# Kernel optimization log

Measured on AMD Instinct MI355X. Metric: run time of the kernel, lower is better.

## Reference

```python
import jax, jax.numpy as jnp
import numpy as np

N = 100000   # num_nodes
H = 128      # hidden_dim
B = 512      # events per forward (batch_size)
D = 32       # fixed neighbor count (padded neighbor list replaces torch.nonzero(A[u]))
NEG = 5      # num_neg_samples
TD_MAX = 1.0 # train_td_max


def setup_inputs() -> dict:
    key = jax.random.key(0)
    ks = jax.random.split(key, 24)
    s = 1.0 / np.sqrt(H)
    inp = {
        # event-stream data (the `data` tuple of forward)
        "time_bar": jax.random.uniform(ks[0], (B, N), dtype=jnp.float32),
        "time_cur": jax.random.uniform(ks[1], (B,), dtype=jnp.float32) + 1.0,
        "time_delta": jax.random.uniform(ks[2], (B, 2), dtype=jnp.float32),
        "u": jax.random.randint(ks[3], (B,), 0, N),
        "neighbors": jax.random.randint(ks[4], (B, D), 0, N),
        "neg_nodes": jax.random.randint(ks[5], (B, NEG), 0, N),
        # recurrent state
        "z0": 0.1 * jax.random.normal(ks[6], (N, H), dtype=jnp.float32),
        # parameters (Linear stored as [in,out] + bias)
        "W_omega": s * jax.random.normal(ks[7], (H,), dtype=jnp.float32),
        "b_omega": jnp.zeros((), jnp.float32),
        "W_h": s * jax.random.normal(ks[8], (H, H), dtype=jnp.float32),
        "b_h": jnp.zeros((H,), jnp.float32),
        "W_e2n": s * jax.random.normal(ks[9], (H, H), dtype=jnp.float32),
        "b_e2n": jnp.zeros((H,), jnp.float32),
        "W_rec_e": s * jax.random.normal(ks[10], (H, H), dtype=jnp.float32),
        "b_rec_e": jnp.zeros((H,), jnp.float32),
        "W_rec_n": s * jax.random.normal(ks[11], (H, H), dtype=jnp.float32),
        "b_rec_n": jnp.zeros((H,), jnp.float32),
        "W_time": s * jax.random.normal(ks[12], (H,), dtype=jnp.float32),
        "b_time": jnp.zeros((H,), jnp.float32),
        "w_t": jnp.full((), 0.5, jnp.float32),
        "alpha": jnp.full((), 0.5, jnp.float32),
        "psi": jnp.full((), 0.5, jnp.float32),
    }
    return inp


def _hawkes(z_u, td, W_omega, b_omega, w_t, alpha, psi):
    # g = omega(z_u); lambda = psi * softplus((g + alpha*exp(-w_t*td)) / psi)
    g = z_u @ W_omega + b_omega                       # [n]
    g = g + alpha * jnp.exp(-w_t * (td / TD_MAX))     # Hawkes time decay
    return psi * jax.nn.softplus(g / psi)             # [n]


def reference(time_bar, time_cur, time_delta, u, neighbors, neg_nodes, z0,
              W_omega, b_omega, W_h, b_h, W_e2n, b_e2n, W_rec_e, b_rec_e,
              W_rec_n, b_rec_n, W_time, b_time, w_t, alpha, psi):
    def step(z, xs):
        u_it, nb_it, tb_it, tc_it, neg_it = xs
        # td for impact nodes: positional indexing into time_bar_it (as in source)
        td = tc_it - tb_it[: 1 + D]                    # [1+D]
        z_u = z[u_it]                                  # [H]  (z_prev row)
        z_nb = z[nb_it]                                # [D,H]
        emb_u = z_u                                    # z_prev[u_event]
        emb_neg = z[neg_it]                            # [NEG,H] z_prev[negatives]
        td_neg = tc_it - tb_it[neg_it]                 # [NEG]
        # recurrent node-embedding update (update_node_embedding_without_attention)
        t_feat = td[:, None] * W_time[None, :] + b_time            # [1+D,H]
        h_u = jax.nn.sigmoid(jnp.mean(z_nb, 0) @ W_h + b_h
                             + z_u @ W_rec_e + b_rec_e + t_feat[0])
        h_nb = jax.nn.sigmoid((z_u @ W_e2n + b_e2n)[None, :]
                              + z_nb @ W_rec_n + b_rec_n + t_feat[1:])
        z = z.at[u_it].set(h_u)
        z = z.at[nb_it].set(h_nb)
        return z, (emb_u, emb_neg, td_neg)

    z_final, (emb_u, emb_neg, td_neg) = jax.lax.scan(
        step, z0, (u, neighbors, time_bar, time_cur, neg_nodes))

    # batch Hawkes intensities on pre-update embeddings
    ts_diff = time_cur - time_delta[:, 0]                           # [B]
    lam = _hawkes(emb_u, ts_diff, W_omega, b_omega, w_t, alpha, psi)          # [B]
    lam_neg = _hawkes(emb_neg.reshape(-1, H), td_neg.reshape(-1),
                      W_omega, b_omega, w_t, alpha, psi)                      # [B*NEG]
    return lam, lam_neg / NEG
```

## Files before the change

kernel.cpp:

```cpp
#include <hip/hip_runtime.h>
#include <stdint.h>

#define NND 100000
#define HD  128
#define BB  512
#define DD  32
#define NNEG 5
#define CAP 12
#define ZROW 132
#define SENT 0xAAAAAAAAu

#define OFF_WCNT     0
#define OFF_WSTEPS   400000
#define OFF_DEP      5200000
#define OFF_STEPOUT  5277824

__global__ void build_writers(const int* __restrict__ u,
                              const int* __restrict__ nb,
                              int* __restrict__ wcnt,
                              int* __restrict__ wsteps) {
    int id = blockIdx.x * blockDim.x + threadIdx.x;
    if (id >= BB * 33) return;
    int s = id / 33, slot = id % 33;
    int row = (slot == 0) ? u[s] : nb[s * DD + slot - 1];
    int pos = atomicAdd(&wcnt[row], 1);
    if (pos < CAP) wsteps[row * CAP + pos] = s * 64 + slot;
}

__global__ void build_deps(const int* __restrict__ u,
                           const int* __restrict__ nb,
                           const int* __restrict__ neg,
                           const int* __restrict__ wcnt,
                           const int* __restrict__ wsteps,
                           int* __restrict__ dep) {
    int id = blockIdx.x * blockDim.x + threadIdx.x;
    if (id >= BB * 38) return;
    int t = id / 38, i = id % 38;
    int row = (i == 0) ? u[t] : (i < 33) ? nb[t * DD + i - 1]
                                         : neg[t * NNEG + i - 33];
    int lim = t * 64;
    int best = -1;
    int n = wcnt[row]; if (n > CAP) n = CAP;
    for (int p = 0; p < n; p++) {
        int e = wsteps[row * CAP + p];
        if (e < lim && e > best) best = e;
    }
    dep[id] = best;
}

__device__ __forceinline__ uint32_t mall_load(const uint32_t* p) {
    return __hip_atomic_load(p, __ATOMIC_RELAXED, __HIP_MEMORY_SCOPE_AGENT);
}
__device__ __forceinline__ void mall_store2(float* p, float v0, float v1) {
    uint64_t pk = ((uint64_t)__float_as_uint(v1) << 32) | (uint64_t)__float_as_uint(v0);
    __hip_atomic_store((unsigned long long*)p, (unsigned long long)pk,
                       __ATOMIC_RELAXED, __HIP_MEMORY_SCOPE_AGENT);
}
__device__ __forceinline__ void flag_set(int* f) {
    __hip_atomic_store(f, 1, __ATOMIC_RELEASE, __HIP_MEMORY_SCOPE_WORKGROUP);
}
__device__ __forceinline__ void flag_wait(int* f) {
    while (__hip_atomic_load(f, __ATOMIC_ACQUIRE, __HIP_MEMORY_SCOPE_WORKGROUP) == 0)
        __builtin_amdgcn_s_sleep(1);
}

__global__ __launch_bounds__(512, 4)
void dyrep_main(const float* __restrict__ time_bar,
                const float* __restrict__ time_cur,
                const float* __restrict__ time_delta,
                const int* __restrict__ u,
                const int* __restrict__ nb,
                const int* __restrict__ neg,
                const float* __restrict__ z0,
                const float* __restrict__ W_omega, const float* __restrict__ b_omega,
                const float* __restrict__ W_h,     const float* __restrict__ b_h,
                const float* __restrict__ W_e2n,   const float* __restrict__ b_e2n,
                const float* __restrict__ W_rec_e, const float* __restrict__ b_rec_e,
                const float* __restrict__ W_rec_n, const float* __restrict__ b_rec_n,
                const float* __restrict__ W_time,  const float* __restrict__ b_time,
                const float* __restrict__ w_t_p,   const float* __restrict__ alpha_p,
                const float* __restrict__ psi_p,
                const int* __restrict__ dep,
                float* __restrict__ step_out,
                float* __restrict__ out) {
    __shared__ float zu[HD];
    __shared__ __align__(16) float znb[DD][ZROW];
    __shared__ float psum[8][HD];
    __shared__ float mbuf[HD];
    __shared__ int flag_zu;
    __shared__ int flag_ps[8];

    const int tid  = threadIdx.x;
    const int lane = tid & 63;
    const int wid  = tid >> 6;
    const int t    = blockIdx.x;
    const int c0   = lane * 2;

    if (tid == 0) flag_zu = 0;
    if (tid < 8)  flag_ps[tid] = 0;
    __syncthreads();

    const float tc  = time_cur[t];
    const float cb0 = b_e2n[c0] + b_rec_n[c0] + b_time[c0];
    const float cb1 = b_e2n[c0+1] + b_rec_n[c0+1] + b_time[c0+1];
    const float wt0 = W_time[c0], wt1 = W_time[c0+1];
    float td_r[4];
    #pragma unroll
    for (int r = 0; r < 4; r++)
        td_r[r] = tc - time_bar[(size_t)t * NND + (1 + 4*wid + r)];

    float cbu0=0.f, cbu1=0.f, td0=0.f, wo0=0.f, wo1=0.f, wt=0.f, al=0.f, ps=0.f, bom=0.f;
    float tdv[6];
    int   negdep[5]; const float* negsrc[5];
    if (wid == 0) {
        cbu0 = b_h[c0] + b_rec_e[c0] + b_time[c0];
        cbu1 = b_h[c0+1] + b_rec_e[c0+1] + b_time[c0+1];
        td0  = tc - time_bar[(size_t)t * NND + 0];
        wo0  = W_omega[c0]; wo1 = W_omega[c0+1];
        wt = *w_t_p; al = *alpha_p; ps = *psi_p; bom = *b_omega;
        tdv[0] = tc - time_delta[t * 2 + 0];
        #pragma unroll
        for (int d = 0; d < 5; d++) {
            int nn = neg[t * NNEG + d];
            tdv[1 + d] = tc - time_bar[(size_t)t * NND + nn];
            int dv = negdep[d] = dep[t * 38 + 33 + d];
            negsrc[d] = (dv >= 0)
                ? step_out + (size_t)(dv >> 6) * 33 * HD + (size_t)(dv & 63) * HD
                : z0 + (size_t)nn * HD;
        }
    }

    if (wid == 0) {
        int d = dep[t * 38 + 0];
        const float* src = (d >= 0)
            ? step_out + (size_t)(d >> 6) * 33 * HD + (size_t)(d & 63) * HD
            : z0 + (size_t)u[t] * HD;
        if (lane < 32) {
            const float* sp = src + lane * 4;
            float4 v;
            if (d >= 0) {
                const uint32_t* ip = (const uint32_t*)sp;
                uint32_t x0, x1, x2, x3;
                while (true) {
                    x0 = mall_load(ip+0); x1 = mall_load(ip+1);
                    x2 = mall_load(ip+2); x3 = mall_load(ip+3);
                    if (x0 != SENT && x1 != SENT && x2 != SENT && x3 != SENT) break;
                    __builtin_amdgcn_s_sleep(1);
                }
                v = make_float4(__uint_as_float(x0), __uint_as_float(x1),
                                __uint_as_float(x2), __uint_as_float(x3));
            } else {
                v = *(const float4*)sp;
            }
            *(float4*)&zu[lane * 4] = v;
        }
        __threadfence_block();
        if (lane == 0) flag_set(&flag_zu);
    }

    {
        const uint32_t* pollp[2]; int lofs[2]; float4 direct[2];
        unsigned pend = 0;
        #pragma unroll
        for (int q = 0; q < 2; q++) {
            int idx = lane + q * 64;
            int rl = idx >> 5, c4 = idx & 31;
            int j = 4 * wid + rl;
            int d = dep[t * 38 + 1 + j];
            const float* sp = (d >= 0)
                ? step_out + (size_t)(d >> 6) * 33 * HD + (size_t)(d & 63) * HD
                : z0 + (size_t)nb[t * DD + j] * HD;
            sp += c4 * 4;
            lofs[q] = j * ZROW + c4 * 4;
            if (d >= 0) { pollp[q] = (const uint32_t*)sp; pend |= (1u << q); }
            else direct[q] = *(const float4*)sp;
        }
        float* zflat = &znb[0][0];
        #pragma unroll
        for (int q = 0; q < 2; q++)
            if (!((pend >> q) & 1)) *(float4*)&zflat[lofs[q]] = direct[q];
        while (__ballot(pend != 0) != 0ULL) {
            #pragma unroll
            for (int q = 0; q < 2; q++) {
                if ((pend >> q) & 1) {
                    const uint32_t* ip = pollp[q];
                    uint32_t x0 = mall_load(ip+0), x1 = mall_load(ip+1);
                    uint32_t x2 = mall_load(ip+2), x3 = mall_load(ip+3);
                    if (x0 != SENT && x1 != SENT && x2 != SENT && x3 != SENT) {
                        *(float4*)&zflat[lofs[q]] =
                            make_float4(__uint_as_float(x0), __uint_as_float(x1),
                                        __uint_as_float(x2), __uint_as_float(x3));
                        pend &= ~(1u << q);
                    }
                }
            }
            if (pend) __builtin_amdgcn_s_sleep(1);
        }
    }
    __threadfence_block();

    {
        float s0 = 0.f, s1 = 0.f;
        #pragma unroll
        for (int r = 0; r < 4; r++) {
            float2 zz = *(const float2*)&znb[4*wid + r][c0];
            s0 += zz.x; s1 += zz.y;
        }
        psum[wid][c0] = s0; psum[wid][c0+1] = s1;
        if (lane == 0) flag_set(&flag_ps[wid]);
        else __builtin_amdgcn_s_sleep(0);
    }

    float2 acc[4];
    #pragma unroll
    for (int r = 0; r < 4; r++) { acc[r].x = 0.f; acc[r].y = 0.f; }
    {
        const float* zr[4];
        #pragma unroll
        for (int r = 0; r < 4; r++) zr[r] = &znb[4*wid + r][0];
        float4 zA[4], zB[4]; float2 wA[4], wB[4];
        #pragma unroll
        for (int r = 0; r < 4; r++) zA[r] = *(const float4*)&zr[r][0];
        #pragma unroll
        for (int kk = 0; kk < 4; kk++) wA[kk] = *(const float2*)&W_rec_n[(size_t)kk * HD + c0];
        for (int kb = 0; kb < HD; kb += 8) {
            #pragma unroll
            for (int r = 0; r < 4; r++) zB[r] = *(const float4*)&zr[r][kb + 4];
            #pragma unroll
            for (int kk = 0; kk < 4; kk++)
                wB[kk] = *(const float2*)&W_rec_n[(size_t)(kb + 4 + kk) * HD + c0];
            #pragma unroll
            for (int r = 0; r < 4; r++) {
                const float za[4] = {zA[r].x, zA[r].y, zA[r].z, zA[r].w};
                #pragma unroll
                for (int kk = 0; kk < 4; kk++) {
                    acc[r].x = fmaf(za[kk], wA[kk].x, acc[r].x);
                    acc[r].y = fmaf(za[kk], wA[kk].y, acc[r].y);
                }
            }
            if (kb + 8 < HD) {
                #pragma unroll
                for (int r = 0; r < 4; r++) zA[r] = *(const float4*)&zr[r][kb + 8];
                #pragma unroll
                for (int kk = 0; kk < 4; kk++)
                    wA[kk] = *(const float2*)&W_rec_n[(size_t)(kb + 8 + kk) * HD + c0];
            }
            #pragma unroll
            for (int r = 0; r < 4; r++) {
                const float zb[4] = {zB[r].x, zB[r].y, zB[r].z, zB[r].w};
                #pragma unroll
                for (int kk = 0; kk < 4; kk++) {
                    acc[r].x = fmaf(zb[kk], wB[kk].x, acc[r].x);
                    acc[r].y = fmaf(zb[kk], wB[kk].y, acc[r].y);
                }
            }
        }
    }

    flag_wait(&flag_zu);
    float e0 = 0.f, e1 = 0.f;
    {
        float4 zA = *(const float4*)&zu[0];
        float2 wA[4], wB[4]; float4 zB;
        #pragma unroll
        for (int kk = 0; kk < 4; kk++) wA[kk] = *(const float2*)&W_e2n[(size_t)kk * HD + c0];
        for (int kb = 0; kb < HD; kb += 8) {
            zB = *(const float4*)&zu[kb + 4];
            #pragma unroll
            for (int kk = 0; kk < 4; kk++)
                wB[kk] = *(const float2*)&W_e2n[(size_t)(kb + 4 + kk) * HD + c0];
            const float za[4] = {zA.x, zA.y, zA.z, zA.w};
            #pragma unroll
            for (int kk = 0; kk < 4; kk++) {
                e0 = fmaf(za[kk], wA[kk].x, e0);
                e1 = fmaf(za[kk], wA[kk].y, e1);
            }
            if (kb + 8 < HD) {
                zA = *(const float4*)&zu[kb + 8];
                #pragma unroll
                for (int kk = 0; kk < 4; kk++)
                    wA[kk] = *(const float2*)&W_e2n[(size_t)(kb + 8 + kk) * HD + c0];
            }
            const float zb[4] = {zB.x, zB.y, zB.z, zB.w};
            #pragma unroll
            for (int kk = 0; kk < 4; kk++) {
                e0 = fmaf(zb[kk], wB[kk].x, e0);
                e1 = fmaf(zb[kk], wB[kk].y, e1);
            }
        }
    }
    float* my_out = step_out + (size_t)t * 33 * HD;
    #pragma unroll
    for (int r = 0; r < 4; r++) {
        int j = 4 * wid + r;
        float p0 = acc[r].x + e0 + td_r[r] * wt0 + cb0;
        float p1 = acc[r].y + e1 + td_r[r] * wt1 + cb1;
        mall_store2(&my_out[(size_t)(1 + j) * HD + c0],
                    1.f / (1.f + __expf(-p0)), 1.f / (1.f + __expf(-p1)));
    }

    if (wid != 0) return;

    #pragma unroll
    for (int g = 0; g < 8; g++) flag_wait(&flag_ps[g]);
    {
        float m0 = 0.f, m1 = 0.f;
        #pragma unroll
        for (int g = 0; g < 8; g++) { m0 += psum[g][c0]; m1 += psum[g][c0+1]; }
        mbuf[c0] = m0 * (1.f/32.f); mbuf[c0+1] = m1 * (1.f/32.f);
    }
    __threadfence_block();
    {
        float a0 = 0.f, a1 = 0.f;
        for (int kb = 0; kb < HD; kb += 4) {
            float4 mv = *(const float4*)&mbuf[kb];
            float4 zv = *(const float4*)&zu[kb];
            const float mm[4] = {mv.x, mv.y, mv.z, mv.w};
            const float zz[4] = {zv.x, zv.y, zv.z, zv.w};
            #pragma unroll
            for (int kk = 0; kk < 4; kk++) {
                float2 wh = *(const float2*)&W_h[(size_t)(kb + kk) * HD + c0];
                float2 wr = *(const float2*)&W_rec_e[(size_t)(kb + kk) * HD + c0];
                a0 = fmaf(mm[kk], wh.x, fmaf(zz[kk], wr.x, a0));
                a1 = fmaf(mm[kk], wh.y, fmaf(zz[kk], wr.y, a1));
            }
        }
        float p0 = a0 + td0 * wt0 + cbu0;
        float p1 = a1 + td0 * wt1 + cbu1;
        mall_store2(&my_out[c0], 1.f / (1.f + __expf(-p0)), 1.f / (1.f + __expf(-p1)));
    }

    {
        float v = zu[c0] * wo0 + zu[c0+1] * wo1;
        #pragma unroll
        for (int off = 32; off; off >>= 1) v += __shfl_down(v, off);
        if (lane == 0) {
            float g = v + bom + al * __expf(-wt * tdv[0]);
            float x = g / ps;
            out[t] = ps * (fmaxf(x, 0.f) + log1pf(__expf(-fabsf(x))));
        }
        for (int d = 0; d < 5; d++) {
            const float* sp = negsrc[d] + c0;
            float x0, x1;
            if (negdep[d] >= 0) {
                const uint32_t* ip = (const uint32_t*)sp;
                uint32_t a, b;
                while (true) {
                    a = mall_load(ip + 0); b = mall_load(ip + 1);
                    if (a != SENT && b != SENT) break;
                    __builtin_amdgcn_s_sleep(1);
                }
                x0 = __uint_as_float(a); x1 = __uint_as_float(b);
            } else {
                x0 = sp[0]; x1 = sp[1];
            }
            float v2 = x0 * wo0 + x1 * wo1;
            #pragma unroll
            for (int off = 32; off; off >>= 1) v2 += __shfl_down(v2, off);
            if (lane == 0) {
                float g = v2 + bom + al * __expf(-wt * tdv[1 + d]);
                float x = g / ps;
                out[BB + t * NNEG + d] =
                    ps * (fmaxf(x, 0.f) + log1pf(__expf(-fabsf(x)))) * (1.0f / NNEG);
            }
        }
    }
}

extern "C" void kernel_launch(void* const* d_in, const int* in_sizes, int n_in,
                              void* d_out, int out_size, void* d_ws, size_t ws_size,
                              hipStream_t stream) {
    const float* time_bar  = (const float*)d_in[0];
    const float* time_cur  = (const float*)d_in[1];
    const float* time_delta= (const float*)d_in[2];
    const int*   u         = (const int*)d_in[3];
    const int*   nb        = (const int*)d_in[4];
    const int*   neg       = (const int*)d_in[5];
    const float* z0        = (const float*)d_in[6];
    const float* W_omega   = (const float*)d_in[7];
    const float* b_omega   = (const float*)d_in[8];
    const float* W_h       = (const float*)d_in[9];
    const float* b_h       = (const float*)d_in[10];
    const float* W_e2n     = (const float*)d_in[11];
    const float* b_e2n     = (const float*)d_in[12];
    const float* W_rec_e   = (const float*)d_in[13];
    const float* b_rec_e   = (const float*)d_in[14];
    const float* W_rec_n   = (const float*)d_in[15];
    const float* b_rec_n   = (const float*)d_in[16];
    const float* W_time    = (const float*)d_in[17];
    const float* b_time    = (const float*)d_in[18];
    const float* w_t       = (const float*)d_in[19];
    const float* alpha     = (const float*)d_in[20];
    const float* psi       = (const float*)d_in[21];

    char* ws = (char*)d_ws;
    int*   wcnt     = (int*)(ws + OFF_WCNT);
    int*   wsteps   = (int*)(ws + OFF_WSTEPS);
    int*   dep      = (int*)(ws + OFF_DEP);
    float* step_out = (float*)(ws + OFF_STEPOUT);
    float* out      = (float*)d_out;

    hipMemsetAsync(ws + OFF_WCNT, 0, NND * 4, stream);
    hipMemsetAsync(ws + OFF_STEPOUT, 0xAA, (size_t)BB * 33 * HD * 4, stream);
    build_writers<<<(BB * 33 + 255) / 256, 256, 0, stream>>>(u, nb, wcnt, wsteps);
    build_deps<<<(BB * 38 + 255) / 256, 256, 0, stream>>>(u, nb, neg, wcnt, wsteps, dep);
    dyrep_main<<<BB, 512, 0, stream>>>(time_bar, time_cur, time_delta, u, nb, neg, z0,
                                       W_omega, b_omega, W_h, b_h, W_e2n, b_e2n,
                                       W_rec_e, b_rec_e, W_rec_n, b_rec_n,
                                       W_time, b_time, w_t, alpha, psi,
                                       dep, step_out, out);
}
```

Measured before the change: 387.9 us.

## Process neighbor rows as they become ready in a polling dataflow loop

Each wave now works through an event loop instead of waiting for all four neighbor rows and z_u before any matvec. Whenever a neighbor row's dependency has been published, the wave runs that row's W_rec_n dot, and it publishes outputs as soon as the W_e2n term is available. This lets downstream blocks start earlier along the dependency chain. The matvecs are also restructured into a shared helper with deeper weight prefetch, at the cost of more registers, per-row weight re-reads (W_rec_n streamed once per row instead of shared across four rows), and more ballot and polling overhead.

```diff
diff --git a/kernel.cpp b/kernel.cpp
--- a/kernel.cpp
+++ b/kernel.cpp
@@ -59,9 +59,44 @@
 __device__ __forceinline__ void flag_set(int* f) {
     __hip_atomic_store(f, 1, __ATOMIC_RELEASE, __HIP_MEMORY_SCOPE_WORKGROUP);
 }
+__device__ __forceinline__ int flag_peek(int* f) {
+    return __hip_atomic_load(f, __ATOMIC_ACQUIRE, __HIP_MEMORY_SCOPE_WORKGROUP);
+}
 __device__ __forceinline__ void flag_wait(int* f) {
-    while (__hip_atomic_load(f, __ATOMIC_ACQUIRE, __HIP_MEMORY_SCOPE_WORKGROUP) == 0)
-        __builtin_amdgcn_s_sleep(1);
+    while (!flag_peek(f)) __builtin_amdgcn_s_sleep(1);
+}
+__device__ __forceinline__ float sigf(float x) {
+    return 1.f / (1.f + __expf(-x));
+}
+
+__device__ __forceinline__ float2 dot_w2(const float* __restrict__ W, int c0,
+                                         const float* __restrict__ zrow) {
+    float a0 = 0.f, a1 = 0.f;
+    float2 wb0[8], wb1[8];
+    #pragma unroll
+    for (int j = 0; j < 8; j++) wb0[j] = *(const float2*)&W[(size_t)j * HD + c0];
+    #pragma unroll
+    for (int kb = 0; kb < HD; kb += 16) {
+        #pragma unroll
+        for (int j = 0; j < 8; j++)
+            wb1[j] = *(const float2*)&W[(size_t)(kb + 8 + j) * HD + c0];
+        #pragma unroll
+        for (int j = 0; j < 8; j++) {
+            float z = zrow[kb + j];
+            a0 = fmaf(z, wb0[j].x, a0); a1 = fmaf(z, wb0[j].y, a1);
+        }
+        if (kb + 16 < HD) {
+            #pragma unroll
+            for (int j = 0; j < 8; j++)
+                wb0[j] = *(const float2*)&W[(size_t)(kb + 16 + j) * HD + c0];
+        }
+        #pragma unroll
+        for (int j = 0; j < 8; j++) {
+            float z = zrow[kb + 8 + j];
+            a0 = fmaf(z, wb1[j].x, a0); a1 = fmaf(z, wb1[j].y, a1);
+        }
+    }
+    return make_float2(a0, a1);
 }
 
 __global__ __launch_bounds__(512, 4)
@@ -101,7 +136,7 @@
     __syncthreads();
 
     const float tc  = time_cur[t];
-    const float cb0 = b_e2n[c0] + b_rec_n[c0] + b_time[c0];
+    const float cb0 = b_e2n[c0]   + b_rec_n[c0]   + b_time[c0];
     const float cb1 = b_e2n[c0+1] + b_rec_n[c0+1] + b_time[c0+1];
     const float wt0 = W_time[c0], wt1 = W_time[c0+1];
     float td_r[4];
@@ -113,7 +148,7 @@
     float tdv[6];
     int   negdep[5]; const float* negsrc[5];
     if (wid == 0) {
-        cbu0 = b_h[c0] + b_rec_e[c0] + b_time[c0];
+        cbu0 = b_h[c0]   + b_rec_e[c0]   + b_time[c0];
         cbu1 = b_h[c0+1] + b_rec_e[c0+1] + b_time[c0+1];
         td0  = tc - time_bar[(size_t)t * NND + 0];
         wo0  = W_omega[c0]; wo1 = W_omega[c0+1];
@@ -130,174 +165,134 @@
         }
     }
 
+    float* zflat = &znb[0][0];
+    const uint32_t* pollp[2]; int lofs[2]; bool done[2];
+    {
+        #pragma unroll
+        for (int q = 0; q < 2; q++) {
+            int rl = q * 2 + (lane >> 5);
+            int j  = 4 * wid + rl;
+            int d  = dep[t * 38 + 1 + j];
+            const float* sp = (d >= 0)
+                ? step_out + (size_t)(d >> 6) * 33 * HD + (size_t)(d & 63) * HD
+                : z0 + (size_t)nb[t * DD + j] * HD;
+            sp += (lane & 31) * 4;
+            lofs[q] = j * ZROW + (lane & 31) * 4;
+            if (d >= 0) { pollp[q] = (const uint32_t*)sp; done[q] = false; }
+            else { *(float4*)&zflat[lofs[q]] = *(const float4*)sp; done[q] = true;
+                   pollp[q] = nullptr; }
+        }
+    }
+
+    const uint32_t* zup = nullptr;
+    bool zu_seg_done = true;
+    bool zu_staged = (wid != 0);
     if (wid == 0) {
         int d = dep[t * 38 + 0];
         const float* src = (d >= 0)
             ? step_out + (size_t)(d >> 6) * 33 * HD + (size_t)(d & 63) * HD
             : z0 + (size_t)u[t] * HD;
-        if (lane < 32) {
-            const float* sp = src + lane * 4;
-            float4 v;
-            if (d >= 0) {
-                const uint32_t* ip = (const uint32_t*)sp;
-                uint32_t x0, x1, x2, x3;
-                while (true) {
-                    x0 = mall_load(ip+0); x1 = mall_load(ip+1);
-                    x2 = mall_load(ip+2); x3 = mall_load(ip+3);
-                    if (x0 != SENT && x1 != SENT && x2 != SENT && x3 != SENT) break;
-                    __builtin_amdgcn_s_sleep(1);
+        if (d < 0) {
+            if (lane < 32) *(float4*)&zu[lane * 4] = *(const float4*)(src + lane * 4);
+            __threadfence_block();
+            if (lane == 0) flag_set(&flag_zu);
+            zu_staged = true;
+        } else {
+            if (lane < 32) { zup = (const uint32_t*)(src + lane * 4); zu_seg_done = false; }
+        }
+    }
+    __threadfence_block();
+
+    float* my_out = step_out + (size_t)t * 33 * HD;
+    float e0 = 0.f, e1 = 0.f;
+    bool e2n_done = false;
+    float2 racc[4];
+    unsigned dotmask = 0, pubmask = 0;
+    float s0 = 0.f, s1 = 0.f;
+
+    while (pubmask != 0xFu) {
+        bool progress = false;
+
+        if (!zu_staged) {
+            if (!zu_seg_done) {
+                uint32_t x0 = mall_load(zup+0), x1 = mall_load(zup+1);
+                uint32_t x2 = mall_load(zup+2), x3 = mall_load(zup+3);
+                if (x0 != SENT && x1 != SENT && x2 != SENT && x3 != SENT) {
+                    *(float4*)&zu[lane * 4] =
+                        make_float4(__uint_as_float(x0), __uint_as_float(x1),
+                                    __uint_as_float(x2), __uint_as_float(x3));
+                    zu_seg_done = true;
                 }
-                v = make_float4(__uint_as_float(x0), __uint_as_float(x1),
-                                __uint_as_float(x2), __uint_as_float(x3));
-            } else {
-                v = *(const float4*)sp;
-            }
-            *(float4*)&zu[lane * 4] = v;
+            }
+            __threadfence_block();
+            unsigned long long bz = __ballot(zu_seg_done);
+            if (bz == ~0ULL) {
+                if (lane == 0) flag_set(&flag_zu);
+                zu_staged = true;
+                progress = true;
+            }
+        }
+
+        if (!e2n_done && flag_peek(&flag_zu)) {
+            float2 ee = dot_w2(W_e2n, c0, zu);
+            e0 = ee.x; e1 = ee.y;
+            e2n_done = true;
+            progress = true;
+        }
+
+        #pragma unroll
+        for (int q = 0; q < 2; q++) {
+            if (!done[q]) {
+                const uint32_t* ip = pollp[q];
+                uint32_t x0 = mall_load(ip+0), x1 = mall_load(ip+1);
+                uint32_t x2 = mall_load(ip+2), x3 = mall_load(ip+3);
+                if (x0 != SENT && x1 != SENT && x2 != SENT && x3 != SENT) {
+                    *(float4*)&zflat[lofs[q]] =
+                        make_float4(__uint_as_float(x0), __uint_as_float(x1),
+                                    __uint_as_float(x2), __uint_as_float(x3));
+                    done[q] = true;
+                }
+            }
         }
         __threadfence_block();
-        if (lane == 0) flag_set(&flag_zu);
-    }
-
-    {
-        const uint32_t* pollp[2]; int lofs[2]; float4 direct[2];
-        unsigned pend = 0;
-        #pragma unroll
-        for (int q = 0; q < 2; q++) {
-            int idx = lane + q * 64;
-            int rl = idx >> 5, c4 = idx & 31;
-            int j = 4 * wid + rl;
-            int d = dep[t * 38 + 1 + j];
-            const float* sp = (d >= 0)
-                ? step_out + (size_t)(d >> 6) * 33 * HD + (size_t)(d & 63) * HD
-                : z0 + (size_t)nb[t * DD + j] * HD;
-            sp += c4 * 4;
-            lofs[q] = j * ZROW + c4 * 4;
-            if (d >= 0) { pollp[q] = (const uint32_t*)sp; pend |= (1u << q); }
-            else direct[q] = *(const float4*)sp;
-        }
-        float* zflat = &znb[0][0];
-        #pragma unroll
-        for (int q = 0; q < 2; q++)
-            if (!((pend >> q) & 1)) *(float4*)&zflat[lofs[q]] = direct[q];
-        while (__ballot(pend != 0) != 0ULL) {
-            #pragma unroll
-            for (int q = 0; q < 2; q++) {
-                if ((pend >> q) & 1) {
-                    const uint32_t* ip = pollp[q];
-                    uint32_t x0 = mall_load(ip+0), x1 = mall_load(ip+1);
-                    uint32_t x2 = mall_load(ip+2), x3 = mall_load(ip+3);
-                    if (x0 != SENT && x1 != SENT && x2 != SENT && x3 != SENT) {
-                        *(float4*)&zflat[lofs[q]] =
-                            make_float4(__uint_as_float(x0), __uint_as_float(x1),
-                                        __uint_as_float(x2), __uint_as_float(x3));
-                        pend &= ~(1u << q);
-                    }
-                }
-            }
-            if (pend) __builtin_amdgcn_s_sleep(1);
-        }
-    }
-    __threadfence_block();
-
-    {
-        float s0 = 0.f, s1 = 0.f;
+
+        unsigned long long b0 = __ballot(done[0]);
+        unsigned long long b1 = __ballot(done[1]);
+        bool ready[4] = { (b0 & 0xFFFFFFFFull) == 0xFFFFFFFFull,
+                          (b0 >> 32)           == 0xFFFFFFFFull,
+                          (b1 & 0xFFFFFFFFull) == 0xFFFFFFFFull,
+                          (b1 >> 32)           == 0xFFFFFFFFull };
+
         #pragma unroll
         for (int r = 0; r < 4; r++) {
-            float2 zz = *(const float2*)&znb[4*wid + r][c0];
-            s0 += zz.x; s1 += zz.y;
-        }
-        psum[wid][c0] = s0; psum[wid][c0+1] = s1;
-        if (lane == 0) flag_set(&flag_ps[wid]);
-        else __builtin_amdgcn_s_sleep(0);
-    }
-
-    float2 acc[4];
-    #pragma unroll
-    for (int r = 0; r < 4; r++) { acc[r].x = 0.f; acc[r].y = 0.f; }
-    {
-        const float* zr[4];
-        #pragma unroll
-        for (int r = 0; r < 4; r++) zr[r] = &znb[4*wid + r][0];
-        float4 zA[4], zB[4]; float2 wA[4], wB[4];
-        #pragma unroll
-        for (int r = 0; r < 4; r++) zA[r] = *(const float4*)&zr[r][0];
-        #pragma unroll
-        for (int kk = 0; kk < 4; kk++) wA[kk] = *(const float2*)&W_rec_n[(size_t)kk * HD + c0];
-        for (int kb = 0; kb < HD; kb += 8) {
-            #pragma unroll
-            for (int r = 0; r < 4; r++) zB[r] = *(const float4*)&zr[r][kb + 4];
-            #pragma unroll
-            for (int kk = 0; kk < 4; kk++)
-                wB[kk] = *(const float2*)&W_rec_n[(size_t)(kb + 4 + kk) * HD + c0];
+            if (ready[r] && !((dotmask >> r) & 1u)) {
+                const float* zr = &znb[4*wid + r][0];
+                racc[r] = dot_w2(W_rec_n, c0, zr);
+                float2 zz = *(const float2*)&zr[c0];
+                s0 += zz.x; s1 += zz.y;
+                dotmask |= 1u << r;
+                progress = true;
+            }
+        }
+        if (e2n_done) {
+            unsigned todo = dotmask & ~pubmask;
             #pragma unroll
             for (int r = 0; r < 4; r++) {
-                const float za[4] = {zA[r].x, zA[r].y, zA[r].z, zA[r].w};
-                #pragma unroll
-                for (int kk = 0; kk < 4; kk++) {
-                    acc[r].x = fmaf(za[kk], wA[kk].x, acc[r].x);
-                    acc[r].y = fmaf(za[kk], wA[kk].y, acc[r].y);
+                if ((todo >> r) & 1u) {
+                    float p0 = racc[r].x + e0 + td_r[r] * wt0 + cb0;
+                    float p1 = racc[r].y + e1 + td_r[r] * wt1 + cb1;
+                    mall_store2(&my_out[(size_t)(1 + 4*wid + r) * HD + c0],
+                                sigf(p0), sigf(p1));
                 }
             }
-            if (kb + 8 < HD) {
-                #pragma unroll
-                for (int r = 0; r < 4; r++) zA[r] = *(const float4*)&zr[r][kb + 8];
-                #pragma unroll
-                for (int kk = 0; kk < 4; kk++)
-                    wA[kk] = *(const float2*)&W_rec_n[(size_t)(kb + 8 + kk) * HD + c0];
-            }
-            #pragma unroll
-            for (int r = 0; r < 4; r++) {
-                const float zb[4] = {zB[r].x, zB[r].y, zB[r].z, zB[r].w};
-                #pragma unroll
-                for (int kk = 0; kk < 4; kk++) {
-                    acc[r].x = fmaf(zb[kk], wB[kk].x, acc[r].x);
-                    acc[r].y = fmaf(zb[kk], wB[kk].y, acc[r].y);
-                }
-            }
-        }
-    }
-
-    flag_wait(&flag_zu);
-    float e0 = 0.f, e1 = 0.f;
-    {
-        float4 zA = *(const float4*)&zu[0];
-        float2 wA[4], wB[4]; float4 zB;
-        #pragma unroll
-        for (int kk = 0; kk < 4; kk++) wA[kk] = *(const float2*)&W_e2n[(size_t)kk * HD + c0];
-        for (int kb = 0; kb < HD; kb += 8) {
-            zB = *(const float4*)&zu[kb + 4];
-            #pragma unroll
-            for (int kk = 0; kk < 4; kk++)
-                wB[kk] = *(const float2*)&W_e2n[(size_t)(kb + 4 + kk) * HD + c0];
-            const float za[4] = {zA.x, zA.y, zA.z, zA.w};
-            #pragma unroll
-            for (int kk = 0; kk < 4; kk++) {
-                e0 = fmaf(za[kk], wA[kk].x, e0);
-                e1 = fmaf(za[kk], wA[kk].y, e1);
-            }
-            if (kb + 8 < HD) {
-                zA = *(const float4*)&zu[kb + 8];
-                #pragma unroll
-                for (int kk = 0; kk < 4; kk++)
-                    wA[kk] = *(const float2*)&W_e2n[(size_t)(kb + 8 + kk) * HD + c0];
-            }
-            const float zb[4] = {zB.x, zB.y, zB.z, zB.w};
-            #pragma unroll
-            for (int kk = 0; kk < 4; kk++) {
-                e0 = fmaf(zb[kk], wB[kk].x, e0);
-                e1 = fmaf(zb[kk], wB[kk].y, e1);
-            }
-        }
-    }
-    float* my_out = step_out + (size_t)t * 33 * HD;
-    #pragma unroll
-    for (int r = 0; r < 4; r++) {
-        int j = 4 * wid + r;
-        float p0 = acc[r].x + e0 + td_r[r] * wt0 + cb0;
-        float p1 = acc[r].y + e1 + td_r[r] * wt1 + cb1;
-        mall_store2(&my_out[(size_t)(1 + j) * HD + c0],
-                    1.f / (1.f + __expf(-p0)), 1.f / (1.f + __expf(-p1)));
-    }
+            pubmask = dotmask;
+        }
+        if (!progress && pubmask != 0xFu) __builtin_amdgcn_s_sleep(1);
+    }
+
+    psum[wid][c0] = s0; psum[wid][c0+1] = s1;
+    __threadfence_block();
+    if (lane == 0) flag_set(&flag_ps[wid]);
 
     if (wid != 0) return;
 
@@ -311,23 +306,11 @@
     }
     __threadfence_block();
     {
-        float a0 = 0.f, a1 = 0.f;
-        for (int kb = 0; kb < HD; kb += 4) {
-            float4 mv = *(const float4*)&mbuf[kb];
-            float4 zv = *(const float4*)&zu[kb];
-            const float mm[4] = {mv.x, mv.y, mv.z, mv.w};
-            const float zz[4] = {zv.x, zv.y, zv.z, zv.w};
-            #pragma unroll
-            for (int kk = 0; kk < 4; kk++) {
-                float2 wh = *(const float2*)&W_h[(size_t)(kb + kk) * HD + c0];
-                float2 wr = *(const float2*)&W_rec_e[(size_t)(kb + kk) * HD + c0];
-                a0 = fmaf(mm[kk], wh.x, fmaf(zz[kk], wr.x, a0));
-                a1 = fmaf(mm[kk], wh.y, fmaf(zz[kk], wr.y, a1));
-            }
-        }
-        float p0 = a0 + td0 * wt0 + cbu0;
-        float p1 = a1 + td0 * wt1 + cbu1;
-        mall_store2(&my_out[c0], 1.f / (1.f + __expf(-p0)), 1.f / (1.f + __expf(-p1)));
+        float2 ah = dot_w2(W_h, c0, mbuf);
+        float2 ar = dot_w2(W_rec_e, c0, zu);
+        float p0 = ah.x + ar.x + td0 * wt0 + cbu0;
+        float p1 = ah.y + ar.y + td0 * wt1 + cbu1;
+        mall_store2(&my_out[c0], sigf(p0), sigf(p1));
     }
 
     {
```

New measurement: 984.3 us. 2.54x slower.
